# Optimization experiments

Hardware: AMD Instinct MI355X
Metric: run time of the kernel (lower is better)

The kernel has to match this reference:

```python
import jax, jax.numpy as jnp
import numpy as np

N_NODES = 50000
N_EDGES = 800000
IN_CH = 128
HEADS = 4
HEAD_DIM = 32  # out_channels // heads = 128 // 4
OUT_CH = HEADS * HEAD_DIM
NEG_SLOPE = 0.2
LN_EPS = 1e-5


def setup_inputs() -> dict:
    key = jax.random.key(0)
    ks = jax.random.split(key, 10)
    s = 1.0 / np.sqrt(IN_CH)
    return {
        "x": jax.random.normal(ks[0], (N_NODES, IN_CH), jnp.float32),
        "edge_index": jax.random.randint(ks[1], (2, N_EDGES), 0, N_NODES, dtype=jnp.int64),
        "W_l": jax.random.normal(ks[2], (IN_CH, OUT_CH), jnp.float32) * s,
        "b_l": jnp.zeros((OUT_CH,), jnp.float32),
        "W_r": jax.random.normal(ks[3], (IN_CH, OUT_CH), jnp.float32) * s,
        "b_r": jnp.zeros((OUT_CH,), jnp.float32),
        "att": jax.random.normal(ks[4], (HEADS, HEAD_DIM), jnp.float32) * (1.0 / np.sqrt(HEAD_DIM)),
        "bias": jnp.zeros((OUT_CH,), jnp.float32),
        "gamma": jnp.ones((OUT_CH,), jnp.float32),
        "beta": jnp.zeros((OUT_CH,), jnp.float32),
    }


def reference(x, edge_index, W_l, b_l, W_r, b_r, att, bias, gamma, beta):
    N = x.shape[0]
    H, C = att.shape
    # add self loops (PyG GATv2Conv default add_self_loops=True)
    loops = jnp.arange(N, dtype=edge_index.dtype)
    src = jnp.concatenate([edge_index[0], loops])  # source j
    dst = jnp.concatenate([edge_index[1], loops])  # target i
    # separate source/target transforms (share_weights=False)
    xl = (x @ W_l + b_l).reshape(N, H, C)  # source features
    xr = (x @ W_r + b_r).reshape(N, H, C)  # target features
    # GATv2 attention: e_ij = att . leaky_relu(xl_j + xr_i)
    e = xl[src] + xr[dst]                              # [E', H, C]
    e = jnp.where(e > 0, e, NEG_SLOPE * e)             # leaky_relu(0.2)
    score = jnp.einsum('ehc,hc->eh', e, att)           # [E', H]
    # segment softmax over edges sharing the same destination node
    smax = jax.ops.segment_max(score, dst, num_segments=N)      # [N, H]
    score = jnp.exp(score - smax[dst])
    denom = jax.ops.segment_sum(score, dst, num_segments=N)     # [N, H]
    alpha = score / denom[dst]                                   # [E', H]
    # weighted scatter-sum of source messages
    msg = alpha[:, :, None] * xl[src]                            # [E', H, C]
    out = jax.ops.segment_sum(msg, dst, num_segments=N)          # [N, H, C]
    out = out.reshape(N, H * C) + bias
    # SiLU
    out = out * jax.nn.sigmoid(out)
    # LayerNorm over feature dim
    mu = jnp.mean(out, axis=-1, keepdims=True)
    var = jnp.mean(jnp.square(out - mu), axis=-1, keepdims=True)
    out = (out - mu) * jax.lax.rsqrt(var + LN_EPS) * gamma + beta
    return out
```

## Files before the change

kernel.cpp:

```cpp
#include <hip/hip_runtime.h>
#include <hip/hip_fp16.h>
#include <math.h>

#define CH 128
#define NEG_SLOPE 0.2f
#define LN_EPS 1e-5f
#define CAP 64

typedef _Float16 f16;
typedef _Float16 f16x2 __attribute__((ext_vector_type(2)));
typedef _Float16 f16x4 __attribute__((ext_vector_type(4)));
typedef _Float16 f16x8 __attribute__((ext_vector_type(8)));
typedef float    f32x4 __attribute__((ext_vector_type(4)));

__device__ __forceinline__ f16x2 u2h(unsigned u) {
    union { unsigned u; f16x2 h; } v; v.u = u; return v.h;
}

__device__ __forceinline__ float row16_allreduce(float x) {
    int t;
    t = __builtin_amdgcn_update_dpp(0, __builtin_bit_cast(int, x), 0xB1, 0xF, 0xF, false);
    x += __builtin_bit_cast(float, t);
    t = __builtin_amdgcn_update_dpp(0, __builtin_bit_cast(int, x), 0x4E, 0xF, 0xF, false);
    x += __builtin_bit_cast(float, t);
    t = __builtin_amdgcn_update_dpp(0, __builtin_bit_cast(int, x), 0x141, 0xF, 0xF, false);
    x += __builtin_bit_cast(float, t);
    t = __builtin_amdgcn_update_dpp(0, __builtin_bit_cast(int, x), 0x140, 0xF, 0xF, false);
    x += __builtin_bit_cast(float, t);
    return x;
}

__global__ void k_init(const float* __restrict__ Wl, const float* __restrict__ Wr,
                       f16* __restrict__ Wt, int* __restrict__ cnt, int N)
{
    int tid = blockIdx.x * 256 + threadIdx.x;
    if (tid < 256 * CH) {
        int k   = tid >> 8;
        int col = tid & 255;
        float w = (col < CH) ? Wl[k * CH + col] : Wr[k * CH + (col - CH)];
        Wt[(size_t)col * CH + k] = (f16)w;
    }
    if (tid < N) cnt[tid] = 0;
}

__global__ __launch_bounds__(256) void k_transform(
    const float* __restrict__ x, const f16* __restrict__ Wt,
    const float* __restrict__ bl, const float* __restrict__ br,
    f16* __restrict__ xlh, f16* __restrict__ xrh, int N)
{
    const int wave = (blockIdx.x * 256 + threadIdx.x) >> 6;
    const int lane = threadIdx.x & 63;
    const int m0   = wave * 16;
    if (m0 >= N) return;

    const int n16  = lane & 15;
    const int quad = lane >> 4;

    f16x8 xfr[4];
    {
        int mrow = m0 + n16; if (mrow >= N) mrow = N - 1;
        const float* xrow = x + (size_t)mrow * CH + quad * 8;
#pragma unroll
        for (int ks = 0; ks < 4; ++ks) {
            float4 p0 = *(const float4*)(xrow + ks * 32);
            float4 p1 = *(const float4*)(xrow + ks * 32 + 4);
            f16x8 f; f[0] = (f16)p0.x; f[1] = (f16)p0.y; f[2] = (f16)p0.z; f[3] = (f16)p0.w;
                     f[4] = (f16)p1.x; f[5] = (f16)p1.y; f[6] = (f16)p1.z; f[7] = (f16)p1.w;
            xfr[ks] = f;
        }
    }

#pragma unroll
    for (int ct = 0; ct < 16; ++ct) {
        f32x4 acc = {0.f, 0.f, 0.f, 0.f};
        const int acol = ct * 16 + n16;
        const f16* wp = Wt + (size_t)acol * CH + quad * 8;
#pragma unroll
        for (int ks = 0; ks < 4; ++ks) {
            f16x8 afr = *(const f16x8*)(wp + ks * 32);
            acc = __builtin_amdgcn_mfma_f32_16x16x32_f16(afr, xfr[ks], acc, 0, 0, 0);
        }
        const int node = m0 + n16;
        const int chq  = ct * 16 + quad * 4;
        if (node < N) {
            if (ct < 8) {
                float4 bv = *(const float4*)&bl[chq];
                f16x4 pk = {(f16)(acc[0] + bv.x), (f16)(acc[1] + bv.y),
                            (f16)(acc[2] + bv.z), (f16)(acc[3] + bv.w)};
                *(f16x4*)(xlh + (size_t)node * CH + chq) = pk;
            } else {
                int cc = chq - CH;
                float4 bv = *(const float4*)&br[cc];
                f16x4 pk = {(f16)(acc[0] + bv.x), (f16)(acc[1] + bv.y),
                            (f16)(acc[2] + bv.z), (f16)(acc[3] + bv.w)};
                *(f16x4*)(xrh + (size_t)node * CH + cc) = pk;
            }
        }
    }
}

__global__ void k_fill(const int* __restrict__ ei, int E,
                       int* __restrict__ cnt, int* __restrict__ col)
{
    int e = blockIdx.x * 256 + threadIdx.x;
    if (e < E) {
        int s = ei[e];
        int d = ei[E + e];
        int pos = atomicAdd(&cnt[d], 1);
        if (pos < CAP) col[((size_t)d << 6) + pos] = s;
    }
}

__global__ __launch_bounds__(256) void k_aggregate(
    const f16* __restrict__ xlh, const f16* __restrict__ xrh,
    const int* __restrict__ col, const int* __restrict__ cnt,
    const float* __restrict__ att, const float* __restrict__ bias,
    const float* __restrict__ gamma, const float* __restrict__ beta,
    float* __restrict__ out, int N)
{
    const int wid  = __builtin_amdgcn_readfirstlane(threadIdx.x >> 6);
    const int lane = threadIdx.x & 63;
    const int n    = blockIdx.x * 4 + wid;
    if (n >= N) return;

    const int start = n << 6;
    int cn = cnt[n]; cn = cn < CAP ? cn : CAP;
    const int end = start + cn;

    const int c = 2 * lane;
    f16x2 xr2, at2;
    {
        xr2 = *(const f16x2*)&xrh[(size_t)n * CH + c];
        float2 a = *(const float2*)&att[c];
        at2 = (f16x2){(f16)(a.x * 1.44269504f), (f16)(a.y * 1.44269504f)};
    }
    const f16x2 c02 = {(f16)NEG_SLOPE, (f16)NEG_SLOPE};
    const unsigned laneoff = (unsigned)c;

    float l_run, accx, accy;
    {
        unsigned us = *(const unsigned*)(xlh + ((size_t)n << 7) + laneoff);
        f16x2 u  = u2h(us);
        f16x2 tt = u + xr2;
        f16x2 lk = __builtin_elementwise_max(tt, tt * c02);
        float s  = __builtin_amdgcn_fdot2(lk, at2, 0.f, false);
        s = row16_allreduce(s);
        float w;
        asm("v_exp_f32 %0, %1" : "=v"(w) : "v"(s));
        l_run = w;
        accx  = (float)u[0] * w;
        accy  = (float)u[1] * w;
    }

    int cc[8];
#pragma unroll
    for (int k = 0; k < 8; ++k) cc[k] = col[start + k];

    for (int p = start; p < end; p += 8) {
        unsigned gv[8];
#pragma unroll
        for (int k = 0; k < 8; ++k) {
            unsigned si = (unsigned)cc[k];
            si = (si < (unsigned)N) ? si : 0u;
            gv[k] = *(const unsigned*)(xlh + ((size_t)si << 7) + laneoff);
        }
#pragma unroll
        for (int k = 0; k < 8; ++k) cc[k] = col[p + 8 + k];
#pragma unroll
        for (int k = 0; k < 8; ++k) {
            f16x2 u  = u2h(gv[k]);
            f16x2 tt = u + xr2;
            f16x2 lk = __builtin_elementwise_max(tt, tt * c02);
            float s  = __builtin_amdgcn_fdot2(lk, at2, 0.f, false);
            s = row16_allreduce(s);
            float w;
            asm("v_exp_f32 %0, %1" : "=v"(w) : "v"(s));
            w = (p + k < end) ? w : 0.f;
            l_run += w;
            accx += (float)u[0] * w;
            accy += (float)u[1] * w;
        }
    }

    const float inv = 1.f / l_run;
    float y0 = accx * inv + bias[c];
    float y1 = accy * inv + bias[c + 1];
    y0 = y0 / (1.f + __expf(-y0));
    y1 = y1 / (1.f + __expf(-y1));
    float s1 = y0 + y1;
    float s2 = y0 * y0 + y1 * y1;
#pragma unroll
    for (int off = 1; off < 64; off <<= 1) {
        s1 += __shfl_xor(s1, off);
        s2 += __shfl_xor(s2, off);
    }
    float mu   = s1 * (1.f / 128.f);
    float var  = s2 * (1.f / 128.f) - mu * mu;
    float rstd = rsqrtf(var + LN_EPS);
    float o0 = (y0 - mu) * rstd * gamma[c]     + beta[c];
    float o1 = (y1 - mu) * rstd * gamma[c + 1] + beta[c + 1];
    *(float2*)&out[(size_t)n * CH + c] = make_float2(o0, o1);
}

extern "C" void kernel_launch(void* const* d_in, const int* in_sizes, int n_in,
                              void* d_out, int out_size, void* d_ws, size_t ws_size,
                              hipStream_t stream)
{
    const float* x    = (const float*)d_in[0];
    const int*   ei   = (const int*)  d_in[1];
    const float* Wl   = (const float*)d_in[2];
    const float* bl   = (const float*)d_in[3];
    const float* Wr   = (const float*)d_in[4];
    const float* br   = (const float*)d_in[5];
    const float* att  = (const float*)d_in[6];
    const float* bias = (const float*)d_in[7];
    const float* gam  = (const float*)d_in[8];
    const float* bet  = (const float*)d_in[9];
    float* out = (float*)d_out;

    const int N = in_sizes[0] / CH;
    const int E = in_sizes[1] / 2;

    char* ws = (char*)d_ws;
    size_t off = 0;
    auto carve = [&](size_t bytes) -> char* {
        char* p = ws + off;
        off += (bytes + 255) & ~(size_t)255;
        return p;
    };
    f16* xlh  = (f16*)carve((size_t)N * CH * sizeof(f16));
    f16* xrh  = (f16*)carve((size_t)N * CH * sizeof(f16));
    f16* Wt   = (f16*)carve((size_t)256 * CH * sizeof(f16));
    int* cnt  = (int*)carve((size_t)N * sizeof(int));
    int* col  = (int*)carve(((size_t)N * CAP + 16) * sizeof(int));
    (void)ws_size;

    const int nwaves = (N + 15) / 16;
    const int TB     = (nwaves * 64 + 255) / 256;
    const int IB     = (((N > 256 * CH ? N : 256 * CH) + 255) / 256);

    k_init      <<<IB, 256, 0, stream>>>(Wl, Wr, Wt, cnt, N);
    k_transform <<<TB, 256, 0, stream>>>(x, Wt, bl, br, xlh, xrh, N);
    k_fill      <<<(E + 255) / 256, 256, 0, stream>>>(ei, E, cnt, col);
    k_aggregate <<<(N + 3) / 4, 256, 0, stream>>>(xlh, xrh, col, cnt,
                                                  att, bias, gam, bet, out, N);
}
```

Before: 216.6 us.

## Partition edge fill kernel by destination class to localize atomics

The CSR fill kernel now launches eight blocks per slice of 4096 edges. Each block reads the edges with int4 vector loads but only performs atomics and column writes for destinations whose node-range class (computed via a multiply-high) matches its block class. This is meant to concentrate atomic and scatter traffic into smaller address ranges per block, which may improve cache or L2 locality. In exchange, every block rereads the edge list eight times. The int4 loads also assume E is a multiple of 4 and that the ei offsets are aligned.

```diff
diff --git a/kernel.cpp b/kernel.cpp
--- a/kernel.cpp
+++ b/kernel.cpp
@@ -99,15 +99,32 @@
     }
 }
 
-__global__ void k_fill(const int* __restrict__ ei, int E,
-                       int* __restrict__ cnt, int* __restrict__ col)
-{
-    int e = blockIdx.x * 256 + threadIdx.x;
-    if (e < E) {
-        int s = ei[e];
-        int d = ei[E + e];
-        int pos = atomicAdd(&cnt[d], 1);
-        if (pos < CAP) col[((size_t)d << 6) + pos] = s;
+#define FILL_EPB 4096
+__global__ __launch_bounds__(256) void k_fill(
+    const int* __restrict__ ei, int E, unsigned CM,
+    int* __restrict__ cnt, int* __restrict__ col)
+{
+    const int cls = blockIdx.x & 7;
+    const int sl  = blockIdx.x >> 3;
+    const int base = sl * FILL_EPB + threadIdx.x * 4;
+
+#pragma unroll
+    for (int i = 0; i < 4; ++i) {
+        int e = base + i * 1024;
+        if (e < E) {
+            int4 dv = *(const int4*)&ei[E + e];
+            int4 sv = *(const int4*)&ei[e];
+            int dd[4] = {dv.x, dv.y, dv.z, dv.w};
+            int ss[4] = {sv.x, sv.y, sv.z, sv.w};
+#pragma unroll
+            for (int k = 0; k < 4; ++k) {
+                int d = dd[k];
+                if ((int)__umulhi((unsigned)d, CM) == cls) {
+                    int pos = atomicAdd(&cnt[d], 1);
+                    if (pos < CAP) col[((size_t)d << 6) + pos] = ss[k];
+                }
+            }
+        }
     }
 }
 
@@ -239,9 +256,13 @@
     const int TB     = (nwaves * 64 + 255) / 256;
     const int IB     = (((N > 256 * CH ? N : 256 * CH) + 255) / 256);
 
+    const unsigned CM = (unsigned)(((8ULL << 32) + (unsigned)N - 1) / (unsigned)N);
+    const int S  = (E + FILL_EPB - 1) / FILL_EPB;
+    const int FB = 8 * S;
+
     k_init      <<<IB, 256, 0, stream>>>(Wl, Wr, Wt, cnt, N);
     k_transform <<<TB, 256, 0, stream>>>(x, Wt, bl, br, xlh, xrh, N);
-    k_fill      <<<(E + 255) / 256, 256, 0, stream>>>(ei, E, cnt, col);
+    k_fill      <<<FB, 256, 0, stream>>>(ei, E, CM, cnt, col);
     k_aggregate <<<(N + 3) / 4, 256, 0, stream>>>(xlh, xrh, col, cnt,
                                                   att, bias, gam, bet, out, N);
 }
```

Measured after the change: 209.9 us. 1.03x faster.
